# Performance work log

Measured on AMD Instinct MI355X. Metric: run time of the kernel, lower is better.

The kernel has to match this reference:

```python
import jax, jax.numpy as jnp
import numpy as np

N, D, K = 50000, 384, 8
B, NEGO, E = 512, 128, 1024
NEG_INF = -1e9
EPS_G = 1e-4


def setup_inputs() -> dict:
    key = jax.random.key(0)
    k1, k2, k3, k4, k5, k6, k7 = jax.random.split(key, 7)
    text_embedding = jax.random.normal(k1, (N, D), dtype=jnp.float32)
    # virtual init: mean direction + small noise (per __init__); exact init values
    # don't matter for the reference math, a random normal param is equivalent.
    virtual = jax.random.normal(k2, (K, D), dtype=jnp.float32)
    gumbel_noise = jax.random.gumbel(k3, (B, NEGO, NEGO), dtype=jnp.float32)
    idx_batch = jnp.sort(jax.random.randint(k4, (B, NEGO), 0, N, dtype=jnp.int32), axis=1)
    edges_src = jax.random.randint(k5, (B, E), 0, NEGO, dtype=jnp.int32)
    edges_dst = jax.random.randint(k6, (B, E), 0, NEGO, dtype=jnp.int32)
    train_label = jax.random.randint(k7, (B,), 0, 2, dtype=jnp.int32)
    return {
        'text_embedding': text_embedding,
        'virtual': virtual,
        'gumbel_noise': gumbel_noise,
        'idx_batch': idx_batch,
        'edges_src': edges_src,
        'edges_dst': edges_dst,
        'train_label': train_label,
    }


def _l2norm(x, axis=-1):
    return x / jnp.sqrt(jnp.sum(x * x, axis=axis, keepdims=True) + 1e-12)


def _forward(text_embedding, virtual, gumbel_noise, idx_batch, edges_src, edges_dst, train_label):
    emb = _l2norm(text_embedding, axis=1)            # [N, D]
    V = _l2norm(virtual, axis=1)                     # [K, D]
    # remove_projection: x - (x V^T (V V^T + eps I)^{-1}) V
    G = V @ V.T + EPS_G * jnp.eye(K, dtype=V.dtype)  # [K, K]
    coef = jnp.linalg.solve(G, (emb @ V.T).T).T      # [N, K] (G symmetric)
    local = _l2norm(emb - coef @ V, axis=1)          # [N, D]

    batch = local[idx_batch]                         # [B, n, D] gather of ego graphs
    sim = jnp.einsum('bnd,bmd->bnm', batch, batch)   # [B, n, n]
    diag = jnp.eye(NEGO, dtype=bool)
    sim = jnp.where(diag[None], NEG_INF, sim)        # fill_diagonal_(-1e9)
    sim_sub = jax.nn.softmax(sim + gumbel_noise, axis=-1)  # gumbel_softmax, tau=1

    # scatter edge list into dense adjacency per ego graph
    b_idx = jnp.arange(B, dtype=jnp.int32)[:, None]
    adj = jnp.zeros((B, NEGO, NEGO), dtype=sim_sub.dtype).at[b_idx, edges_src, edges_dst].set(1.0)

    # torch.norm(adj - sim_sub, 2, dim=1) on each [n, n] matrix -> reduce axis -1 batched
    diff = jnp.sqrt(jnp.sum((adj - sim_sub) ** 2, axis=2))  # [B, n]
    score = jnp.mean(diff, axis=1)                           # [B]

    score = (score - jnp.min(score)) / (jnp.max(score) - jnp.min(score) + 1e-8)
    y = train_label.astype(score.dtype)
    logp = jnp.maximum(jnp.log(score), -100.0)      # BCELoss clamps log at -100
    log1mp = jnp.maximum(jnp.log1p(-score), -100.0)
    loss = -jnp.mean(y * logp + (1.0 - y) * log1mp)
    return score, loss


def reference(text_embedding, virtual, gumbel_noise, idx_batch, edges_src, edges_dst, train_label):
    return _forward(text_embedding, virtual, gumbel_noise, idx_batch, edges_src, edges_dst, train_label)
```

## Files before the change

### kernel.cpp

```cpp
#include <hip/hip_runtime.h>
#include <hip/hip_bf16.h>
#include <stdint.h>

#define N_ROWS 50000
#define D 384
#define K 8
#define BATCH 512
#define NEGO 128
#define NEDGE 1024
#define EPS_G 1e-4f

typedef float f32x4 __attribute__((ext_vector_type(4)));
typedef short bf16x8 __attribute__((ext_vector_type(8)));

__device__ __forceinline__ float wave_reduce_sum(float v) {
#pragma unroll
    for (int d = 1; d < 64; d <<= 1) v += __shfl_xor(v, d);
    return v;
}

static __device__ __forceinline__ uint16_t f2bfbits(float f) {
    __hip_bfloat16 h = __float2bfloat16(f);
    union { __hip_bfloat16 h; uint16_t u; } cv;
    cv.h = h;
    return cv.u;
}

__global__ __launch_bounds__(64) void prep_kernel(const float* __restrict__ virt,
                                                  float* __restrict__ Vn,
                                                  float* __restrict__ Ginv,
                                                  float* __restrict__ M1,
                                                  uint16_t* __restrict__ Vbf) {
    __shared__ float Vs[K * D];
    __shared__ float As[K * K];
    __shared__ float Is[K * K];
    int tid = threadIdx.x;
    for (int t = tid; t < K * D; t += 64) Vs[t] = virt[t];
    __syncthreads();
    for (int k = 0; k < K; ++k) {
        float ss = 0.f;
        for (int t = tid; t < D; t += 64) { float v = Vs[k * D + t]; ss += v * v; }
        ss = wave_reduce_sum(ss);
        float inv = 1.0f / sqrtf(ss + 1e-12f);
        for (int t = tid; t < D; t += 64) {
            float v = Vs[k * D + t] * inv;
            Vs[k * D + t] = v;
            Vn[k * D + t] = v;
        }
        __syncthreads();
    }
    int k = tid >> 3, m = tid & 7;
    {
        const f32x4* a4 = (const f32x4*)&Vs[k * D];
        const f32x4* b4 = (const f32x4*)&Vs[m * D];
        float g = 0.f;
        for (int j = 0; j < 96; ++j) {
            f32x4 a = a4[j], b = b4[j];
            g += a.x * b.x + a.y * b.y + a.z * b.z + a.w * b.w;
        }
        if (k == m) g += EPS_G;
        As[tid] = g;
        Is[tid] = (k == m) ? 1.f : 0.f;
    }
    __syncthreads();
#pragma unroll
    for (int p = 0; p < K; ++p) {
        float piv = 1.0f / As[p * K + p];
        if (k == p) { As[tid] *= piv; Is[tid] *= piv; }
        __syncthreads();
        float f = As[k * K + p];
        float ap = As[p * K + m], ip = Is[p * K + m];
        __syncthreads();
        if (k != p) { As[tid] -= f * ap; Is[tid] -= f * ip; }
        __syncthreads();
    }
    {
        float gi = Is[tid];
        Ginv[tid] = gi;
        float q = 0.f;
#pragma unroll
        for (int c = 0; c < K; ++c) q += Is[k * K + c] * Is[c * K + m];
        M1[tid] = gi + EPS_G * q;
    }
#pragma unroll
    for (int r = 0; r < 16; ++r)
        for (int cj = tid; cj < D; cj += 64)
            Vbf[r * D + cj] = (r < K) ? f2bfbits(Vs[r * D + cj]) : (uint16_t)0;
}

__global__ __launch_bounds__(512) void batch_kernel(const float* __restrict__ emb,
                                                    const float* __restrict__ gumbel,
                                                    const int* __restrict__ idx_batch,
                                                    const int* __restrict__ edges_src,
                                                    const int* __restrict__ edges_dst,
                                                    const __hip_bfloat16* __restrict__ Vbf,
                                                    const float* __restrict__ M1,
                                                    float* __restrict__ scores) {
    __shared__ __hip_bfloat16 Xs[NEGO * D];
    __shared__ uint32_t adjmask[NEGO * 4];
    __shared__ int idxs[NEGO];
    __shared__ float Yl[NEGO][12];
    __shared__ float Al[NEGO][12];
    __shared__ float diagL[NEGO];
    __shared__ float invrL[NEGO];
    __shared__ float red[8];
    int tid = threadIdx.x;
    int b = blockIdx.x;
    if (tid < NEGO) idxs[tid] = idx_batch[b * NEGO + tid];
    adjmask[tid] = 0u;
    __syncthreads();

    {
        int row = tid >> 2, seg = tid & 3;
        const f32x4* src = (const f32x4*)(emb + (size_t)idxs[row] * D);
        f32x4 xt[24];
#pragma unroll
        for (int i = 0; i < 24; ++i) xt[i] = src[seg + 4 * i];
        char* db = (char*)Xs;
#pragma unroll
        for (int i = 0; i < 24; ++i) {
            int j = seg + 4 * i;
            ushort4 p;
            p.x = f2bfbits(xt[i].x); p.y = f2bfbits(xt[i].y);
            p.z = f2bfbits(xt[i].z); p.w = f2bfbits(xt[i].w);
            int off = (row * 768 + j * 8) ^ ((row & 7) << 4);
            *(ushort4*)(db + off) = p;
        }
    }
    for (int e = tid; e < NEDGE; e += 512) {
        int s = edges_src[b * NEDGE + e];
        int dd = edges_dst[b * NEDGE + e];
        atomicOr(&adjmask[s * 4 + (dd >> 5)], 1u << (dd & 31));
    }
    __syncthreads();

    int w = tid >> 6, l = tid & 63;
    int c15 = l & 15, g4 = l >> 4;

    float gpre[4][8];
    {
        const float* gb = gumbel + (size_t)b * NEGO * NEGO;
#pragma unroll
        for (int reg = 0; reg < 4; ++reg) {
            int row = w * 16 + g4 * 4 + reg;
#pragma unroll
            for (int t = 0; t < 8; ++t) gpre[reg][t] = gb[row * NEGO + 16 * t + c15];
        }
    }

    f32x4 acc[8];
    f32x4 accY = (f32x4){0.f, 0.f, 0.f, 0.f};
#pragma unroll
    for (int t = 0; t < 8; ++t) acc[t] = (f32x4){0.f, 0.f, 0.f, 0.f};
    const char* xb = (const char*)Xs;
    int ar = w * 16 + c15;
    int aswz = (ar & 7) << 4;
    for (int ks = 0; ks < 12; ++ks) {
        int kbyte = ks * 64 + g4 * 16;
        bf16x8 afrag = *(const bf16x8*)(xb + ((ar * 768 + kbyte) ^ aswz));
        bf16x8 vfrag = *(const bf16x8*)(Vbf + (size_t)c15 * D + ks * 32 + g4 * 8);
        accY = __builtin_amdgcn_mfma_f32_16x16x32_bf16(afrag, vfrag, accY, 0, 0, 0);
#pragma unroll
        for (int t = 0; t < 8; ++t) {
            int br = t * 16 + c15;
            bf16x8 bfrag = *(const bf16x8*)(xb + ((br * 768 + kbyte) ^ ((br & 7) << 4)));
            acc[t] = __builtin_amdgcn_mfma_f32_16x16x32_bf16(afrag, bfrag, acc[t], 0, 0, 0);
        }
    }

#pragma unroll
    for (int reg = 0; reg < 4; ++reg) {
        int row = w * 16 + g4 * 4 + reg;
        if (c15 < 8) Yl[row][c15] = accY[reg];
#pragma unroll
        for (int t = 0; t < 8; ++t)
            if (t == w && c15 == g4 * 4 + reg) diagL[row] = acc[t][reg];
    }
    __syncthreads();

    if (tid < NEGO) {
        float y[K], a[K];
#pragma unroll
        for (int kk = 0; kk < K; ++kk) y[kk] = Yl[tid][kk];
        float crr = 0.f;
#pragma unroll
        for (int kk = 0; kk < K; ++kk) {
            float s = 0.f;
#pragma unroll
            for (int mm = 0; mm < K; ++mm) s += y[mm] * M1[mm * K + kk];
            a[kk] = s;
            crr += s * y[kk];
        }
#pragma unroll
        for (int kk = 0; kk < K; ++kk) Al[tid][kk] = a[kk];
        invrL[tid] = 1.0f / sqrtf(diagL[tid] - crr + 1e-12f);
    }
    __syncthreads();

    float wave_score = 0.f;
#pragma unroll
    for (int reg = 0; reg < 4; ++reg) {
        int row = w * 16 + g4 * 4 + reg;
        const f32x4* ar4 = (const f32x4*)&Al[row][0];
        f32x4 a0 = ar4[0], a1 = ar4[1];
        float invr = invrL[row];
        float z[8];
#pragma unroll
        for (int t = 0; t < 8; ++t) {
            int col = 16 * t + c15;
            const f32x4* yc4 = (const f32x4*)&Yl[col][0];
            f32x4 y0 = yc4[0], y1 = yc4[1];
            float corr = a0.x * y0.x + a0.y * y0.y + a0.z * y0.z + a0.w * y0.w +
                         a1.x * y1.x + a1.y * y1.y + a1.z * y1.z + a1.w * y1.w;
            float s = (acc[t][reg] - corr) * invr * invrL[col];
            if (col == row) s = -1e9f;
            z[t] = s + gpre[reg][t];
        }
        float m = z[0];
#pragma unroll
        for (int t = 1; t < 8; ++t) m = fmaxf(m, z[t]);
#pragma unroll
        for (int d = 1; d < 16; d <<= 1) m = fmaxf(m, __shfl_xor(m, d));
        float e[8], se = 0.f;
#pragma unroll
        for (int t = 0; t < 8; ++t) { e[t] = expf(z[t] - m); se += e[t]; }
#pragma unroll
        for (int d = 1; d < 16; d <<= 1) se += __shfl_xor(se, d);
        float inv = 1.0f / se;
        uint32_t am[4];
#pragma unroll
        for (int qq = 0; qq < 4; ++qq) am[qq] = adjmask[row * 4 + qq];
        float sq = 0.f;
#pragma unroll
        for (int t = 0; t < 8; ++t) {
            int col = 16 * t + c15;
            float a = (float)((am[col >> 5] >> (col & 31)) & 1u);
            float d0 = a - e[t] * inv;
            sq += d0 * d0;
        }
#pragma unroll
        for (int d = 1; d < 16; d <<= 1) sq += __shfl_xor(sq, d);
        wave_score += sqrtf(sq);
    }
    wave_score += __shfl_xor(wave_score, 16);
    wave_score += __shfl_xor(wave_score, 32);
    if (l == 0) red[w] = wave_score;
    __syncthreads();
    if (tid == 0) {
        float tot = 0.f;
#pragma unroll
        for (int ww = 0; ww < 8; ++ww) tot += red[ww];
        scores[b] = tot * (1.0f / (float)NEGO);
    }
}

__global__ __launch_bounds__(512) void finalize_kernel(const float* __restrict__ scores,
                                                       const int* __restrict__ labels,
                                                       float* __restrict__ out) {
    __shared__ float rmn[8], rmx[8], rsum[8];
    int tid = threadIdx.x, w = tid >> 6, l = tid & 63;
    float s = scores[tid];
    float mn = s, mx = s;
#pragma unroll
    for (int d = 1; d < 64; d <<= 1) {
        mn = fminf(mn, __shfl_xor(mn, d));
        mx = fmaxf(mx, __shfl_xor(mx, d));
    }
    if (l == 0) { rmn[w] = mn; rmx[w] = mx; }
    __syncthreads();
    mn = rmn[0]; mx = rmx[0];
#pragma unroll
    for (int ww = 1; ww < 8; ++ww) {
        mn = fminf(mn, rmn[ww]);
        mx = fmaxf(mx, rmx[ww]);
    }
    float norm = (s - mn) / (mx - mn + 1e-8f);
    out[tid] = norm;
    float y = (float)labels[tid];
    float lp = fmaxf(logf(norm), -100.0f);
    float l1p = fmaxf(log1pf(-norm), -100.0f);
    float term = y * lp + (1.0f - y) * l1p;
    term = wave_reduce_sum(term);
    if (l == 0) rsum[w] = term;
    __syncthreads();
    if (tid == 0) {
        float tot = 0.f;
        for (int ww = 0; ww < 8; ++ww) tot += rsum[ww];
        out[BATCH] = -tot / (float)BATCH;
    }
}

extern "C" void kernel_launch(void* const* d_in, const int* in_sizes, int n_in,
                              void* d_out, int out_size, void* d_ws, size_t ws_size,
                              hipStream_t stream) {
    (void)in_sizes; (void)n_in; (void)out_size; (void)ws_size;
    const float* text = (const float*)d_in[0];
    const float* virt = (const float*)d_in[1];
    const float* gum = (const float*)d_in[2];
    const int* idxb = (const int*)d_in[3];
    const int* esrc = (const int*)d_in[4];
    const int* edst = (const int*)d_in[5];
    const int* label = (const int*)d_in[6];
    float* out = (float*)d_out;

    float* Vn = (float*)d_ws;
    float* Ginv = Vn + K * D;
    float* M1 = Ginv + K * K;
    float* scores = M1 + K * K;
    uint16_t* Vbf = (uint16_t*)(scores + BATCH);

    hipLaunchKernelGGL(prep_kernel, dim3(1), dim3(64), 0, stream, virt, Vn, Ginv, M1, Vbf);
    hipLaunchKernelGGL(batch_kernel, dim3(BATCH), dim3(512), 0, stream, text, gum, idxb,
                       esrc, edst, (const __hip_bfloat16*)Vbf, M1, scores);
    hipLaunchKernelGGL(finalize_kernel, dim3(1), dim3(512), 0, stream, scores, label, out);
}
```

Measured before the change: 63.03 us.

## Stage embedding gather through LDS with direct global-to-LDS loads

```diff
diff --git a/kernel.cpp b/kernel.cpp
--- a/kernel.cpp
+++ b/kernel.cpp
@@ -12,6 +12,7 @@
 
 typedef float f32x4 __attribute__((ext_vector_type(4)));
 typedef short bf16x8 __attribute__((ext_vector_type(8)));
+typedef unsigned short ushort8v __attribute__((ext_vector_type(8)));
 
 __device__ __forceinline__ float wave_reduce_sum(float v) {
 #pragma unroll
@@ -26,9 +27,12 @@
     return cv.u;
 }
 
+__device__ __forceinline__ void gload_lds16(const void* g, void* l) {
+    __builtin_amdgcn_global_load_lds((const __attribute__((address_space(1))) void*)g,
+                                     (__attribute__((address_space(3))) void*)l, 16, 0, 0);
+}
+
 __global__ __launch_bounds__(64) void prep_kernel(const float* __restrict__ virt,
-                                                  float* __restrict__ Vn,
-                                                  float* __restrict__ Ginv,
                                                   float* __restrict__ M1,
                                                   uint16_t* __restrict__ Vbf) {
     __shared__ float Vs[K * D];
@@ -42,11 +46,7 @@
         for (int t = tid; t < D; t += 64) { float v = Vs[k * D + t]; ss += v * v; }
         ss = wave_reduce_sum(ss);
         float inv = 1.0f / sqrtf(ss + 1e-12f);
-        for (int t = tid; t < D; t += 64) {
-            float v = Vs[k * D + t] * inv;
-            Vs[k * D + t] = v;
-            Vn[k * D + t] = v;
-        }
+        for (int t = tid; t < D; t += 64) Vs[k * D + t] *= inv;
         __syncthreads();
     }
     int k = tid >> 3, m = tid & 7;
@@ -75,12 +75,10 @@
         __syncthreads();
     }
     {
-        float gi = Is[tid];
-        Ginv[tid] = gi;
         float q = 0.f;
 #pragma unroll
         for (int c = 0; c < K; ++c) q += Is[k * K + c] * Is[c * K + m];
-        M1[tid] = gi + EPS_G * q;
+        M1[tid] = Is[tid] + EPS_G * q;
     }
 #pragma unroll
     for (int r = 0; r < 16; ++r)
@@ -97,12 +95,9 @@
                                                     const float* __restrict__ M1,
                                                     float* __restrict__ scores) {
     __shared__ __hip_bfloat16 Xs[NEGO * D];
+    __shared__ float Fbuf[12288];
     __shared__ uint32_t adjmask[NEGO * 4];
     __shared__ int idxs[NEGO];
-    __shared__ float Yl[NEGO][12];
-    __shared__ float Al[NEGO][12];
-    __shared__ float diagL[NEGO];
-    __shared__ float invrL[NEGO];
     __shared__ float red[8];
     int tid = threadIdx.x;
     int b = blockIdx.x;
@@ -110,32 +105,52 @@
     adjmask[tid] = 0u;
     __syncthreads();
 
-    {
-        int row = tid >> 2, seg = tid & 3;
-        const f32x4* src = (const f32x4*)(emb + (size_t)idxs[row] * D);
-        f32x4 xt[24];
-#pragma unroll
-        for (int i = 0; i < 24; ++i) xt[i] = src[seg + 4 * i];
-        char* db = (char*)Xs;
-#pragma unroll
-        for (int i = 0; i < 24; ++i) {
-            int j = seg + 4 * i;
-            ushort4 p;
-            p.x = f2bfbits(xt[i].x); p.y = f2bfbits(xt[i].y);
-            p.z = f2bfbits(xt[i].z); p.w = f2bfbits(xt[i].w);
-            int off = (row * 768 + j * 8) ^ ((row & 7) << 4);
-            *(ushort4*)(db + off) = p;
-        }
-    }
+    int l = tid & 63, w = tid >> 6;
+    int c15 = l & 15, g4 = l >> 4;
+
     for (int e = tid; e < NEDGE; e += 512) {
         int s = edges_src[b * NEDGE + e];
         int dd = edges_dst[b * NEDGE + e];
         atomicOr(&adjmask[s * 4 + (dd >> 5)], 1u << (dd & 31));
     }
-    __syncthreads();
-
-    int w = tid >> 6, l = tid & 63;
-    int c15 = l & 15, g4 = l >> 4;
+
+    const char* eb = (const char*)emb;
+    char* fb = (char*)Fbuf;
+#pragma unroll
+    for (int p = 0; p < 4; ++p) {
+#pragma unroll
+        for (int j = 0; j < 6; ++j) {
+            int boff = w * 6144 + j * 1024;
+            int off = boff + l * 16;
+            int rl = off / 1536;
+            int rem = off - rl * 1536;
+            const void* src = eb + (size_t)idxs[p * 32 + rl] * 1536 + rem;
+            gload_lds16(src, fb + boff);
+        }
+        __syncthreads();
+#pragma unroll
+        for (int m = 0; m < 3; ++m) {
+            int chunk = m * 1024 + tid * 2;
+            int rl = chunk / 96;
+            int c2 = chunk - rl * 96;
+            const f32x4* fp = (const f32x4*)(Fbuf + rl * 384 + c2 * 4);
+            f32x4 a = fp[0], bb = fp[1];
+            ushort8v pk;
+            pk[0] = f2bfbits(a.x); pk[1] = f2bfbits(a.y);
+            pk[2] = f2bfbits(a.z); pk[3] = f2bfbits(a.w);
+            pk[4] = f2bfbits(bb.x); pk[5] = f2bfbits(bb.y);
+            pk[6] = f2bfbits(bb.z); pk[7] = f2bfbits(bb.w);
+            int grow = p * 32 + rl;
+            int offb = (grow * 768 + (c2 >> 1) * 16) ^ ((grow & 7) << 4);
+            *(ushort8v*)((char*)Xs + offb) = pk;
+        }
+        __syncthreads();
+    }
+
+    float (*Yl)[12] = (float(*)[12])Fbuf;
+    float (*Al)[12] = (float(*)[12])(Fbuf + 1536);
+    float* diagL = Fbuf + 3072;
+    float* invrL = Fbuf + 3200;
 
     float gpre[4][8];
     {
@@ -303,13 +318,11 @@
     const int* label = (const int*)d_in[6];
     float* out = (float*)d_out;
 
-    float* Vn = (float*)d_ws;
-    float* Ginv = Vn + K * D;
-    float* M1 = Ginv + K * K;
+    float* M1 = (float*)d_ws;
     float* scores = M1 + K * K;
     uint16_t* Vbf = (uint16_t*)(scores + BATCH);
 
-    hipLaunchKernelGGL(prep_kernel, dim3(1), dim3(64), 0, stream, virt, Vn, Ginv, M1, Vbf);
+    hipLaunchKernelGGL(prep_kernel, dim3(1), dim3(64), 0, stream, virt, M1, Vbf);
     hipLaunchKernelGGL(batch_kernel, dim3(BATCH), dim3(512), 0, stream, text, gum, idxb,
                        esrc, edst, (const __hip_bfloat16*)Vbf, M1, scores);
     hipLaunchKernelGGL(finalize_kernel, dim3(1), dim3(512), 0, stream, scores, label, out);
```

New measurement: 63.61 us. Within noise of the previous version (+0.9%).
